# Kernel tuning notes

Measured on AMD Instinct MI355X. Metric: run time of the kernel, lower is better.

## Reference

```python
import jax, jax.numpy as jnp
import numpy as np

NUM_HEADS = 16
HEAD_DIM = 64  # embedding_dim 1024 / 16


def setup_inputs() -> dict:
    key = jax.random.key(0)
    k1, k2, k3, k4 = jax.random.split(key, 4)
    B, S, D = 2, 2048, 1024
    return {
        "query": jax.random.normal(k1, (B, S, D), dtype=jnp.float32),
        "key": jax.random.normal(k2, (B, S, D), dtype=jnp.float32),
        "value": jax.random.normal(k3, (B, S, D), dtype=jnp.float32),
        "W_out": jax.random.normal(k4, (D, D), dtype=jnp.float32) * (1.0 / np.sqrt(D)),
        "b_out": jnp.zeros((D,), dtype=jnp.float32),
    }


def reference(query, key, value, W_out, b_out):
    B, S, D = query.shape
    H, hd = NUM_HEADS, HEAD_DIM
    # NOTE: original forward never applies q_fc/k_fc/v_fc (transform ignores fc)
    q = query.reshape(B, S, H, hd).transpose(0, 2, 1, 3)  # [B,H,S,hd]
    k = key.reshape(B, S, H, hd).transpose(0, 2, 1, 3)
    v = value.reshape(B, S, H, hd).transpose(0, 2, 1, 3)
    scores = jnp.einsum("bhqd,bhkd->bhqk", q, k) / jnp.sqrt(jnp.float32(hd))
    probs = jax.nn.softmax(scores, axis=-1)  # mask=None, dropout=None
    ctx = jnp.einsum("bhqk,bhkd->bhqd", probs, v)
    ctx = ctx.transpose(0, 2, 1, 3).reshape(B, S, D)
    return ctx @ W_out.T + b_out
```

## Files before the change

### kernel.cpp

```cpp
#include <hip/hip_runtime.h>
#include <hip/hip_bf16.h>
#include <stdint.h>

#define NB 2
#define SEQ 2048
#define DIM 1024
#define NH 16
#define HD 64

typedef __attribute__((ext_vector_type(4))) float f32x4;
typedef __attribute__((ext_vector_type(16))) float f32x16;
typedef __attribute__((ext_vector_type(8))) short s16x8;
typedef __attribute__((ext_vector_type(4))) short s16x4;
typedef __attribute__((ext_vector_type(8))) __bf16 bf16x8;

static __device__ __forceinline__ short f2bf_rne(float x) {
  uint32_t u = __float_as_uint(x);
  u += 0x7fffu + ((u >> 16) & 1u);
  return (short)(u >> 16);
}
static __device__ __forceinline__ uint32_t pk_bf16(float a, float b) {
  __hip_bfloat162 h = __float22bfloat162_rn(float2{a, b});
  uint32_t u;
  __builtin_memcpy(&u, &h, 4);
  return u;
}
static __device__ __forceinline__ bf16x8 ldfrag(const short* p) {
  bf16x8 r;
  __builtin_memcpy(&r, p, 16);
  return r;
}
static __device__ __forceinline__ void glds16(const short* g, short* l) {
  __builtin_amdgcn_global_load_lds(
      (const __attribute__((address_space(1))) uint32_t*)g,
      (__attribute__((address_space(3))) uint32_t*)l, 16, 0, 0);
}

__global__ __launch_bounds__(256) void prep_all(const float* __restrict__ K,
                                                const float* __restrict__ V,
                                                const float* __restrict__ W,
                                                short* __restrict__ Kh,
                                                short* __restrict__ Vt,
                                                short* __restrict__ Wh) {
  __shared__ float vtile[64][65];
  const int tid = threadIdx.x;
  const int id = blockIdx.x;

  if (id >= 1024) {
    size_t idx = ((size_t)(id - 1024) * 256 + tid) * 8;
    f32x4 a = *(const f32x4*)(W + idx);
    f32x4 b = *(const f32x4*)(W + idx + 4);
    s16x8 o;
#pragma unroll
    for (int j = 0; j < 4; ++j) {
      o[j] = f2bf_rne(a[j]);
      o[4 + j] = f2bf_rne(b[j]);
    }
    *(s16x8*)(Wh + idx) = o;
    return;
  }

  const int t0 = (id & 31) * 64;
  const int bh = id >> 5;
  const int b = bh >> 4, h = bh & 15;

#pragma unroll
  for (int i = 0; i < 4; ++i) {
    int f = tid + 256 * i;
    int row = f >> 4;
    int col = (f & 15) * 4;
    const float* src = K + ((size_t)(b * SEQ + t0 + row)) * DIM + h * HD + col;
    f32x4 v = *(const f32x4*)src;
    s16x4 hi;
#pragma unroll
    for (int j = 0; j < 4; ++j) hi[j] = f2bf_rne(v[j]);
    *(s16x4*)(Kh + ((size_t)bh * SEQ + t0 + row) * HD + col) = hi;
  }
#pragma unroll
  for (int i = 0; i < 4; ++i) {
    int f = tid + 256 * i;
    int row = f >> 4;
    int col = (f & 15) * 4;
    const float* src = V + ((size_t)(b * SEQ + t0 + row)) * DIM + h * HD + col;
    f32x4 v = *(const f32x4*)src;
#pragma unroll
    for (int j = 0; j < 4; ++j) vtile[row][col + j] = v[j];
  }
  __syncthreads();
#pragma unroll
  for (int i = 0; i < 4; ++i) {
    int idx = tid + 256 * i;
    int d = idx >> 4;
    int kb = (idx & 15) * 4;
    int kp = (kb & ~12) | ((kb & 4) << 1) | ((kb & 8) >> 1);
    s16x4 o4;
#pragma unroll
    for (int j = 0; j < 4; ++j) o4[j] = f2bf_rne(vtile[kb + j][d]);
    *(s16x4*)(Vt + ((size_t)bh * HD + d) * SEQ + t0 + kp) = o4;
  }
}

#define QSCALE (0.125f * 1.44269504088896340736f)

__global__ __launch_bounds__(256, 2) void attn(const float* __restrict__ Q,
                                               const short* __restrict__ Kh,
                                               const short* __restrict__ Vt,
                                               short* __restrict__ Ch) {
  __shared__ __align__(16) short ksh[2][64 * 64];
  __shared__ __align__(16) short vts[2][64 * 64];

  const int tid = threadIdx.x;
  const int wv = tid >> 6, ln = tid & 63;
  const int l32 = ln & 31, hl = ln >> 5;
  const int bh = blockIdx.y, b = bh >> 4, hh = bh & 15;
  const int q0 = blockIdx.x * 128 + wv * 32;

  bf16x8 qh[4];
  {
    const float* qp = Q + ((size_t)(b * SEQ + q0 + l32)) * DIM + hh * HD + hl * 8;
#pragma unroll
    for (int ks = 0; ks < 4; ++ks) {
      short th[8];
#pragma unroll
      for (int j = 0; j < 8; ++j) th[j] = f2bf_rne(qp[ks * 16 + j] * QSCALE);
      __builtin_memcpy(&qh[ks], th, 16);
    }
  }

  f32x16 acc[2];
#pragma unroll
  for (int r = 0; r < 16; ++r) {
    acc[0][r] = 0.f;
    acc[1][r] = 0.f;
  }
  float den0 = 0.f, den1 = 0.f;

  const short* khg = Kh + (size_t)bh * SEQ * HD;
  const short* vtg = Vt + (size_t)bh * HD * SEQ;

  const int srow8 = ln >> 3;
  const int sg = ln & 7;

#pragma unroll
  for (int i = 0; i < 4; ++i) {
    int c = wv * 4 + i;
    int row = (c & 7) * 8 + srow8;
    int sw = (sg ^ srow8) * 8;
    if (c < 8)
      glds16(khg + (size_t)row * HD + sw, &ksh[0][(c & 7) * 512]);
    else
      glds16(vtg + (size_t)row * SEQ + sw, &vts[0][(c & 7) * 512]);
  }

  for (int t = 0; t < SEQ / 64; ++t) {
    __syncthreads();
    if (t + 1 < SEQ / 64) {
      const int kk = (t + 1) * 64;
      const int bn = (t + 1) & 1;
#pragma unroll
      for (int i = 0; i < 4; ++i) {
        int c = wv * 4 + i;
        int row = (c & 7) * 8 + srow8;
        int sw = (sg ^ srow8) * 8;
        if (c < 8)
          glds16(khg + (size_t)(kk + row) * HD + sw, &ksh[bn][(c & 7) * 512]);
        else
          glds16(vtg + (size_t)row * SEQ + kk + sw, &vts[bn][(c & 7) * 512]);
      }
    }
    const short* kb = ksh[t & 1];
    const short* vbuf = vts[t & 1];

#pragma unroll
    for (int nt = 0; nt < 2; ++nt) {
      f32x16 sf;
#pragma unroll
      for (int r = 0; r < 16; ++r) sf[r] = 0.f;
#pragma unroll
      for (int ks = 0; ks < 4; ++ks) {
        bf16x8 kf =
            ldfrag(kb + (nt * 32 + l32) * 64 + (((ks * 2 + hl) ^ (l32 & 7)) * 8));
        sf = __builtin_amdgcn_mfma_f32_32x32x16_bf16(kf, qh[ks], sf, 0, 0, 0);
      }
#pragma unroll
      for (int tp = 0; tp < 2; ++tp) {
        uint32_t w[4];
#pragma unroll
        for (int j2 = 0; j2 < 4; ++j2) {
          float p0 = __builtin_amdgcn_exp2f(sf[tp * 8 + j2 * 2]);
          float p1 = __builtin_amdgcn_exp2f(sf[tp * 8 + j2 * 2 + 1]);
          den0 += p0;
          den1 += p1;
          w[j2] = pk_bf16(p0, p1);
        }
        bf16x8 pa;
        __builtin_memcpy(&pa, w, 16);
        const int ksg = nt * 2 + tp;
#pragma unroll
        for (int dt = 0; dt < 2; ++dt) {
          bf16x8 vf = ldfrag(vbuf + (dt * 32 + l32) * 64 +
                             (((ksg * 2 + hl) ^ (l32 & 7)) * 8));
          acc[dt] =
              __builtin_amdgcn_mfma_f32_32x32x16_bf16(pa, vf, acc[dt], 0, 0, 0);
        }
      }
    }
  }

  float den = den0 + den1;
  den += __shfl_xor(den, 32);
  float invd = 1.0f / den;
  float inv_r[16];
#pragma unroll
  for (int r = 0; r < 16; ++r)
    inv_r[r] = __shfl(invd, (r & 3) + 8 * (r >> 2) + 4 * hl, 64);
#pragma unroll
  for (int dt = 0; dt < 2; ++dt)
#pragma unroll
    for (int r = 0; r < 16; ++r) {
      int row = (r & 3) + 8 * (r >> 2) + 4 * hl;
      size_t off = ((size_t)(b * SEQ + q0 + row)) * DIM + hh * HD + dt * 32 + l32;
      Ch[off] = f2bf_rne(acc[dt][r] * inv_r[r]);
    }
}

__global__ __launch_bounds__(256, 2) void proj(const short* __restrict__ Ah,
                                               const short* __restrict__ Wh,
                                               const float* __restrict__ bias,
                                               float* __restrict__ OUT) {
  __shared__ __align__(16) short ash[2][128 * 64];
  __shared__ __align__(16) short wsh[2][64 * 64];
  const int tid = threadIdx.x;
  const int wv = tid >> 6, ln = tid & 63;
  const int l32 = ln & 31, hl = ln >> 5;
  const int m0 = blockIdx.x * 128, n0 = blockIdx.y * 64;

  f32x16 acc[2];
#pragma unroll
  for (int r = 0; r < 16; ++r) {
    acc[0][r] = 0.f;
    acc[1][r] = 0.f;
  }

  const int srow8 = ln >> 3, sg = ln & 7;

#pragma unroll
  for (int i = 0; i < 6; ++i) {
    int c = wv * 6 + i;
    int sw = (sg ^ srow8) * 8;
    if (c < 16) {
      int row = c * 8 + srow8;
      glds16(Ah + (size_t)(m0 + row) * DIM + sw, &ash[0][c * 512]);
    } else {
      int row = (c - 16) * 8 + srow8;
      glds16(Wh + (size_t)(n0 + row) * DIM + sw, &wsh[0][(c - 16) * 512]);
    }
  }

  for (int kt = 0; kt < DIM / 64; ++kt) {
    __syncthreads();
    if (kt + 1 < DIM / 64) {
      const int kk = (kt + 1) * 64;
      const int bn = (kt + 1) & 1;
#pragma unroll
      for (int i = 0; i < 6; ++i) {
        int c = wv * 6 + i;
        int sw = (sg ^ srow8) * 8;
        if (c < 16) {
          int row = c * 8 + srow8;
          glds16(Ah + (size_t)(m0 + row) * DIM + kk + sw, &ash[bn][c * 512]);
        } else {
          int row = (c - 16) * 8 + srow8;
          glds16(Wh + (size_t)(n0 + row) * DIM + kk + sw, &wsh[bn][(c - 16) * 512]);
        }
      }
    }
    const short* ab = ash[kt & 1];
    const short* wb = wsh[kt & 1];
#pragma unroll
    for (int ks = 0; ks < 4; ++ks) {
      bf16x8 af = ldfrag(ab + (wv * 32 + l32) * 64 + (((ks * 2 + hl) ^ (l32 & 7)) * 8));
#pragma unroll
      for (int nt = 0; nt < 2; ++nt) {
        bf16x8 wf =
            ldfrag(wb + (nt * 32 + l32) * 64 + (((ks * 2 + hl) ^ (l32 & 7)) * 8));
        acc[nt] = __builtin_amdgcn_mfma_f32_32x32x16_bf16(af, wf, acc[nt], 0, 0, 0);
      }
    }
  }

  float bs[2];
#pragma unroll
  for (int nt = 0; nt < 2; ++nt) bs[nt] = bias[n0 + nt * 32 + l32];
#pragma unroll
  for (int nt = 0; nt < 2; ++nt)
#pragma unroll
    for (int r = 0; r < 16; ++r) {
      int row = m0 + wv * 32 + (r & 3) + 8 * (r >> 2) + 4 * hl;
      int col = n0 + nt * 32 + l32;
      OUT[(size_t)row * DIM + col] = acc[nt][r] + bs[nt];
    }
}

extern "C" void kernel_launch(void* const* d_in, const int* in_sizes, int n_in,
                              void* d_out, int out_size, void* d_ws, size_t ws_size,
                              hipStream_t stream) {
  const float* Q = (const float*)d_in[0];
  const float* K = (const float*)d_in[1];
  const float* V = (const float*)d_in[2];
  const float* W = (const float*)d_in[3];
  const float* bias = (const float*)d_in[4];
  float* OUT = (float*)d_out;

  char* ws = (char*)d_ws;
  short* Kh = (short*)(ws + ((size_t)0 << 20));
  short* Vt = (short*)(ws + ((size_t)8 << 20));
  short* Ch = (short*)(ws + ((size_t)16 << 20));
  short* Wh = (short*)(ws + ((size_t)24 << 20));

  prep_all<<<dim3(1536), 256, 0, stream>>>(K, V, W, Kh, Vt, Wh);
  attn<<<dim3(SEQ / 128, NB * NH), 256, 0, stream>>>(Q, Kh, Vt, Ch);
  proj<<<dim3((NB * SEQ) / 128, DIM / 64), 256, 0, stream>>>(Ch, Wh, bias, OUT);
}
```

Before: 162.9 us.

## Split attention KV loop across two wave groups and shrink projection tiles

The attention kernel now launches 512 threads per block. Two groups of four waves each process alternating 64-key tiles, and the partial accumulators and denominators are combined through shared memory at the end. This split-K scheme is meant to raise wave occupancy and latency hiding, since the grid has only 512 blocks. The projection kernel moves to 64x64 tiles with one MFMA accumulator per wave, doubling the block count to improve occupancy. The cost is an extra shared-memory reduction in attention and less operand reuse per wave in the projection.

```diff
diff --git a/kernel.cpp b/kernel.cpp
--- a/kernel.cpp
+++ b/kernel.cpp
@@ -102,18 +102,23 @@
 
 #define QSCALE (0.125f * 1.44269504088896340736f)
 
-__global__ __launch_bounds__(256, 2) void attn(const float* __restrict__ Q,
+__global__ __launch_bounds__(512, 4) void attn(const float* __restrict__ Q,
                                                const short* __restrict__ Kh,
                                                const short* __restrict__ Vt,
                                                short* __restrict__ Ch) {
-  __shared__ __align__(16) short ksh[2][64 * 64];
-  __shared__ __align__(16) short vts[2][64 * 64];
+  __shared__ __align__(16) short smem[32768];
 
   const int tid = threadIdx.x;
   const int wv = tid >> 6, ln = tid & 63;
+  const int grp = wv >> 2, wl = wv & 3;
   const int l32 = ln & 31, hl = ln >> 5;
   const int bh = blockIdx.y, b = bh >> 4, hh = bh & 15;
-  const int q0 = blockIdx.x * 128 + wv * 32;
+  const int q0 = blockIdx.x * 128 + wl * 32;
+
+  short* kt0 = smem + grp * 2 * 4096;
+  short* kt1 = smem + (grp * 2 + 1) * 4096;
+  short* vt0 = smem + 16384 + grp * 2 * 4096;
+  short* vt1 = smem + 16384 + (grp * 2 + 1) * 4096;
 
   bf16x8 qh[4];
   {
@@ -140,36 +145,39 @@
 
   const int srow8 = ln >> 3;
   const int sg = ln & 7;
-
-#pragma unroll
-  for (int i = 0; i < 4; ++i) {
-    int c = wv * 4 + i;
-    int row = (c & 7) * 8 + srow8;
-    int sw = (sg ^ srow8) * 8;
-    if (c < 8)
-      glds16(khg + (size_t)row * HD + sw, &ksh[0][(c & 7) * 512]);
-    else
-      glds16(vtg + (size_t)row * SEQ + sw, &vts[0][(c & 7) * 512]);
-  }
-
-  for (int t = 0; t < SEQ / 64; ++t) {
+  const int sw = (sg ^ srow8) * 8;
+
+  {
+    const int kv0 = grp * 64;
+#pragma unroll
+    for (int i = 0; i < 4; ++i) {
+      int c = wl * 4 + i;
+      int row = (c & 7) * 8 + srow8;
+      if (c < 8)
+        glds16(khg + (size_t)(kv0 + row) * HD + sw, kt0 + (c & 7) * 512);
+      else
+        glds16(vtg + (size_t)row * SEQ + kv0 + sw, vt0 + (c & 7) * 512);
+    }
+  }
+
+  for (int t = 0; t < 16; ++t) {
     __syncthreads();
-    if (t + 1 < SEQ / 64) {
-      const int kk = (t + 1) * 64;
-      const int bn = (t + 1) & 1;
+    if (t + 1 < 16) {
+      const int kvn = (2 * (t + 1) + grp) * 64;
+      short* kd = ((t + 1) & 1) ? kt1 : kt0;
+      short* vd = ((t + 1) & 1) ? vt1 : vt0;
 #pragma unroll
       for (int i = 0; i < 4; ++i) {
-        int c = wv * 4 + i;
+        int c = wl * 4 + i;
         int row = (c & 7) * 8 + srow8;
-        int sw = (sg ^ srow8) * 8;
         if (c < 8)
-          glds16(khg + (size_t)(kk + row) * HD + sw, &ksh[bn][(c & 7) * 512]);
+          glds16(khg + (size_t)(kvn + row) * HD + sw, kd + (c & 7) * 512);
         else
-          glds16(vtg + (size_t)row * SEQ + kk + sw, &vts[bn][(c & 7) * 512]);
-      }
-    }
-    const short* kb = ksh[t & 1];
-    const short* vbuf = vts[t & 1];
+          glds16(vtg + (size_t)row * SEQ + kvn + sw, vd + (c & 7) * 512);
+      }
+    }
+    const short* kb = (t & 1) ? kt1 : kt0;
+    const short* vbuf = (t & 1) ? vt1 : vt0;
 
 #pragma unroll
     for (int nt = 0; nt < 2; ++nt) {
@@ -207,54 +215,76 @@
     }
   }
 
-  float den = den0 + den1;
-  den += __shfl_xor(den, 32);
-  float invd = 1.0f / den;
-  float inv_r[16];
-#pragma unroll
-  for (int r = 0; r < 16; ++r)
-    inv_r[r] = __shfl(invd, (r & 3) + 8 * (r >> 2) + 4 * hl, 64);
-#pragma unroll
-  for (int dt = 0; dt < 2; ++dt)
-#pragma unroll
-    for (int r = 0; r < 16; ++r) {
-      int row = (r & 3) + 8 * (r >> 2) + 4 * hl;
-      size_t off = ((size_t)(b * SEQ + q0 + row)) * DIM + hh * HD + dt * 32 + l32;
-      Ch[off] = f2bf_rne(acc[dt][r] * inv_r[r]);
-    }
-}
-
-__global__ __launch_bounds__(256, 2) void proj(const short* __restrict__ Ah,
+  __syncthreads();
+  f32x4* R4 = (f32x4*)smem;
+  float* Rd = (float*)smem + 8192;
+  if (grp == 1) {
+#pragma unroll
+    for (int dt = 0; dt < 2; ++dt)
+#pragma unroll
+      for (int j = 0; j < 4; ++j) {
+        f32x4 v = {acc[dt][j * 4 + 0], acc[dt][j * 4 + 1], acc[dt][j * 4 + 2],
+                   acc[dt][j * 4 + 3]};
+        R4[(wl * 8 + dt * 4 + j) * 64 + ln] = v;
+      }
+    Rd[wl * 64 + ln] = den0 + den1;
+  }
+  __syncthreads();
+  if (grp == 0) {
+    float den = den0 + den1 + Rd[wl * 64 + ln];
+#pragma unroll
+    for (int dt = 0; dt < 2; ++dt)
+#pragma unroll
+      for (int j = 0; j < 4; ++j) {
+        f32x4 v = R4[(wl * 8 + dt * 4 + j) * 64 + ln];
+#pragma unroll
+        for (int e = 0; e < 4; ++e) acc[dt][j * 4 + e] += v[e];
+      }
+    den += __shfl_xor(den, 32);
+    float invd = 1.0f / den;
+    float inv_r[16];
+#pragma unroll
+    for (int r = 0; r < 16; ++r)
+      inv_r[r] = __shfl(invd, (r & 3) + 8 * (r >> 2) + 4 * hl, 64);
+#pragma unroll
+    for (int dt = 0; dt < 2; ++dt)
+#pragma unroll
+      for (int r = 0; r < 16; ++r) {
+        int row = (r & 3) + 8 * (r >> 2) + 4 * hl;
+        size_t off =
+            ((size_t)(b * SEQ + q0 + row)) * DIM + hh * HD + dt * 32 + l32;
+        Ch[off] = f2bf_rne(acc[dt][r] * inv_r[r]);
+      }
+  }
+}
+
+__global__ __launch_bounds__(256, 4) void proj(const short* __restrict__ Ah,
                                                const short* __restrict__ Wh,
                                                const float* __restrict__ bias,
                                                float* __restrict__ OUT) {
-  __shared__ __align__(16) short ash[2][128 * 64];
-  __shared__ __align__(16) short wsh[2][64 * 64];
+  __shared__ __align__(16) short ash[2][4096];
+  __shared__ __align__(16) short wsh[2][4096];
   const int tid = threadIdx.x;
   const int wv = tid >> 6, ln = tid & 63;
   const int l32 = ln & 31, hl = ln >> 5;
-  const int m0 = blockIdx.x * 128, n0 = blockIdx.y * 64;
-
-  f32x16 acc[2];
-#pragma unroll
-  for (int r = 0; r < 16; ++r) {
-    acc[0][r] = 0.f;
-    acc[1][r] = 0.f;
-  }
+  const int wm = wv & 1, wn = wv >> 1;
+  const int m0 = blockIdx.x * 64, n0 = blockIdx.y * 64;
+
+  f32x16 acc;
+#pragma unroll
+  for (int r = 0; r < 16; ++r) acc[r] = 0.f;
 
   const int srow8 = ln >> 3, sg = ln & 7;
-
-#pragma unroll
-  for (int i = 0; i < 6; ++i) {
-    int c = wv * 6 + i;
-    int sw = (sg ^ srow8) * 8;
-    if (c < 16) {
-      int row = c * 8 + srow8;
-      glds16(Ah + (size_t)(m0 + row) * DIM + sw, &ash[0][c * 512]);
-    } else {
-      int row = (c - 16) * 8 + srow8;
-      glds16(Wh + (size_t)(n0 + row) * DIM + sw, &wsh[0][(c - 16) * 512]);
-    }
+  const int sw = (sg ^ srow8) * 8;
+
+#pragma unroll
+  for (int i = 0; i < 4; ++i) {
+    int c = wv * 4 + i;
+    int row = (c & 7) * 8 + srow8;
+    if (c < 8)
+      glds16(Ah + (size_t)(m0 + row) * DIM + sw, ash[0] + (c & 7) * 512);
+    else
+      glds16(Wh + (size_t)(n0 + row) * DIM + sw, wsh[0] + (c & 7) * 512);
   }
 
   for (int kt = 0; kt < DIM / 64; ++kt) {
@@ -263,43 +293,32 @@
       const int kk = (kt + 1) * 64;
       const int bn = (kt + 1) & 1;
 #pragma unroll
-      for (int i = 0; i < 6; ++i) {
-        int c = wv * 6 + i;
-        int sw = (sg ^ srow8) * 8;
-        if (c < 16) {
-          int row = c * 8 + srow8;
-          glds16(Ah + (size_t)(m0 + row) * DIM + kk + sw, &ash[bn][c * 512]);
-        } else {
-          int row = (c - 16) * 8 + srow8;
-          glds16(Wh + (size_t)(n0 + row) * DIM + kk + sw, &wsh[bn][(c - 16) * 512]);
-        }
+      for (int i = 0; i < 4; ++i) {
+        int c = wv * 4 + i;
+        int row = (c & 7) * 8 + srow8;
+        if (c < 8)
+          glds16(Ah + (size_t)(m0 + row) * DIM + kk + sw, ash[bn] + (c & 7) * 512);
+        else
+          glds16(Wh + (size_t)(n0 + row) * DIM + kk + sw, wsh[bn] + (c & 7) * 512);
       }
     }
     const short* ab = ash[kt & 1];
     const short* wb = wsh[kt & 1];
 #pragma unroll
     for (int ks = 0; ks < 4; ++ks) {
-      bf16x8 af = ldfrag(ab + (wv * 32 + l32) * 64 + (((ks * 2 + hl) ^ (l32 & 7)) * 8));
-#pragma unroll
-      for (int nt = 0; nt < 2; ++nt) {
-        bf16x8 wf =
-            ldfrag(wb + (nt * 32 + l32) * 64 + (((ks * 2 + hl) ^ (l32 & 7)) * 8));
-        acc[nt] = __builtin_amdgcn_mfma_f32_32x32x16_bf16(af, wf, acc[nt], 0, 0, 0);
-      }
-    }
-  }
-
-  float bs[2];
-#pragma unroll
-  for (int nt = 0; nt < 2; ++nt) bs[nt] = bias[n0 + nt * 32 + l32];
-#pragma unroll
-  for (int nt = 0; nt < 2; ++nt)
-#pragma unroll
-    for (int r = 0; r < 16; ++r) {
-      int row = m0 + wv * 32 + (r & 3) + 8 * (r >> 2) + 4 * hl;
-      int col = n0 + nt * 32 + l32;
-      OUT[(size_t)row * DIM + col] = acc[nt][r] + bs[nt];
-    }
+      bf16x8 af = ldfrag(ab + (wm * 32 + l32) * 64 + (((ks * 2 + hl) ^ (l32 & 7)) * 8));
+      bf16x8 wf = ldfrag(wb + (wn * 32 + l32) * 64 + (((ks * 2 + hl) ^ (l32 & 7)) * 8));
+      acc = __builtin_amdgcn_mfma_f32_32x32x16_bf16(af, wf, acc, 0, 0, 0);
+    }
+  }
+
+  float bs = bias[n0 + wn * 32 + l32];
+#pragma unroll
+  for (int r = 0; r < 16; ++r) {
+    int row = m0 + wm * 32 + (r & 3) + 8 * (r >> 2) + 4 * hl;
+    int col = n0 + wn * 32 + l32;
+    OUT[(size_t)row * DIM + col] = acc[r] + bs;
+  }
 }
 
 extern "C" void kernel_launch(void* const* d_in, const int* in_sizes, int n_in,
@@ -319,6 +338,6 @@
   short* Wh = (short*)(ws + ((size_t)24 << 20));
 
   prep_all<<<dim3(1536), 256, 0, stream>>>(K, V, W, Kh, Vt, Wh);
-  attn<<<dim3(SEQ / 128, NB * NH), 256, 0, stream>>>(Q, Kh, Vt, Ch);
-  proj<<<dim3((NB * SEQ) / 128, DIM / 64), 256, 0, stream>>>(Ch, Wh, bias, OUT);
-}
+  attn<<<dim3(SEQ / 128, NB * NH), 512, 0, stream>>>(Q, Kh, Vt, Ch);
+  proj<<<dim3((NB * SEQ) / 64, DIM / 64), 256, 0, stream>>>(Ch, Wh, bias, OUT);
+}
```

After: 162.7 us. Within noise of the previous version (-0.1%).
